# Kernel tuning notes

Hardware: AMD Instinct MI355X
Metric: run time of the kernel (lower is better)

Reference implementation:

```python
import jax, jax.numpy as jnp
import numpy as np

N_NODES = 100000
N_EDGES = 1600000
D_NODE = 96
D_EDGE = 32
N_GRAPHS = 128
BN_EPS = 1e-5


def setup_inputs() -> dict:
    key = jax.random.key(0)
    ks = jax.random.split(key, 8)
    x = jax.random.normal(ks[0], (N_NODES, D_NODE), dtype=jnp.float32)
    edge_attr = jax.random.normal(ks[1], (N_EDGES, D_EDGE), dtype=jnp.float32)
    edge_index = jax.random.randint(ks[2], (2, N_EDGES), 0, N_NODES, dtype=jnp.int64)
    batch = jnp.sort(jax.random.randint(ks[3], (N_NODES,), 0, N_GRAPHS, dtype=jnp.int64))
    W1 = jax.random.normal(ks[4], (16, D_NODE + D_EDGE), dtype=jnp.float32) * 0.09
    b1 = jax.random.normal(ks[5], (16,), dtype=jnp.float32) * 0.01
    gamma = jnp.ones((16,), dtype=jnp.float32)
    beta = jnp.zeros((16,), dtype=jnp.float32)
    run_mean = jnp.zeros((16,), dtype=jnp.float32)
    run_var = jnp.ones((16,), dtype=jnp.float32)
    W2 = jax.random.normal(ks[6], (1, 16), dtype=jnp.float32) * 0.25
    b2 = jax.random.normal(ks[7], (1,), dtype=jnp.float32) * 0.01
    return {"x": x, "edge_attr": edge_attr, "edge_index": edge_index, "batch": batch,
            "W1": W1, "b1": b1, "gamma": gamma, "beta": beta,
            "run_mean": run_mean, "run_var": run_var, "W2": W2, "b2": b2}


def reference(x, edge_attr, edge_index, batch, W1, b1, gamma, beta, run_mean, run_var, W2, b2):
    src, dst = edge_index[0], edge_index[1]
    # per-edge message: MLP(cat([x_j, edge_attr]))  -- [E, d_node+d_edge]
    msg_in = jnp.concatenate([x[src], edge_attr], axis=1)
    h = msg_in @ W1.T + b1                                  # [E, 16]
    # BatchNorm1d in eval mode (running stats); Dropout is identity in eval
    h = gamma * (h - run_mean) * jax.lax.rsqrt(run_var + BN_EPS) + beta
    h = jax.nn.relu(h)
    msg = h @ W2.T + b2                                     # [E, 1]
    # scatter-add messages to target nodes
    node_out = jax.ops.segment_sum(msg, dst, num_segments=N_NODES)   # [N, 1]
    # global add pool per graph
    pooled = jax.ops.segment_sum(node_out, batch, num_segments=N_GRAPHS)  # [G, 1]
    # mean over feature dim (size 1)
    return jnp.mean(pooled, axis=1)                         # [G]
```

## Files before the change

### kernel.cpp

```cpp
#include <hip/hip_runtime.h>

#define N_NODES 100000
#define N_EDGES 1600000
#define D_NODE 96
#define D_EDGE 32
#define N_GRAPHS 128
#define BN_EPS 1e-5f

#define EDGE_BLOCKS 1024
#define EDGE_THREADS 256

__global__ void prep_kernel(const float* __restrict__ W1, const float* __restrict__ b1,
                            const float* __restrict__ gamma, const float* __restrict__ beta,
                            const float* __restrict__ rmean, const float* __restrict__ rvar,
                            const float* __restrict__ W2, const float* __restrict__ b2,
                            float* __restrict__ w1n, float* __restrict__ w1e,
                            float* __restrict__ cw) {
    int t = threadIdx.x;
    if (t < 16) {
        float A = gamma[t] * rsqrtf(rvar[t] + BN_EPS);
        cw[t] = A * (b1[t] - rmean[t]) + beta[t];
        cw[16 + t] = W2[t];
        for (int j = 0; j < D_NODE; ++j)
            w1n[t * D_NODE + j] = A * W1[t * (D_NODE + D_EDGE) + j];
        for (int j = 0; j < D_EDGE; ++j)
            w1e[t * D_EDGE + j] = A * W1[t * (D_NODE + D_EDGE) + D_NODE + j];
    }
    if (t == 16) cw[32] = b2[0];
}

__global__ __launch_bounds__(256) void node_proj_kernel(const float* __restrict__ x,
                                                        const float* __restrict__ w1n,
                                                        float* __restrict__ y) {
    int n = blockIdx.x * 256 + threadIdx.x;
    if (n >= N_NODES) return;
    const float4* xr = (const float4*)(x + (size_t)n * D_NODE);
    float acc[16];
#pragma unroll
    for (int k = 0; k < 16; ++k) acc[k] = 0.f;
#pragma unroll
    for (int j4 = 0; j4 < D_NODE / 4; ++j4) {
        float4 xv = xr[j4];
#pragma unroll
        for (int k = 0; k < 16; ++k) {
            const float* w = w1n + k * D_NODE + j4 * 4;
            acc[k] += xv.x * w[0] + xv.y * w[1] + xv.z * w[2] + xv.w * w[3];
        }
    }
    float4* yr = (float4*)(y + (size_t)n * 16);
#pragma unroll
    for (int q = 0; q < 4; ++q)
        yr[q] = make_float4(acc[q * 4 + 0], acc[q * 4 + 1], acc[q * 4 + 2], acc[q * 4 + 3]);
}

__global__ __launch_bounds__(EDGE_THREADS) void edge_kernel(
    const float* __restrict__ ea, const int* __restrict__ eidx,
    const int* __restrict__ batch, const float* __restrict__ y,
    const float* __restrict__ w1e, const float* __restrict__ cw,
    float* __restrict__ partials) {
    __shared__ float bins[N_GRAPHS];
    int t = threadIdx.x;
    if (t < N_GRAPHS) bins[t] = 0.f;
    __syncthreads();

    const int* srcp = eidx;
    const int* dstp = eidx + N_EDGES;
    float b2v = cw[32];

    for (int e = blockIdx.x * EDGE_THREADS + t; e < N_EDGES; e += EDGE_BLOCKS * EDGE_THREADS) {
        int s = srcp[e];
        int d = dstp[e];

        const float4* er = (const float4*)(ea + (size_t)e * D_EDGE);
        float4 ev[8];
#pragma unroll
        for (int i = 0; i < 8; ++i) ev[i] = er[i];

        float ya[16];
        const float4* yr = (const float4*)(y + (size_t)s * 16);
#pragma unroll
        for (int q = 0; q < 4; ++q) ((float4*)ya)[q] = yr[q];

        float msg = b2v;
#pragma unroll
        for (int k = 0; k < 16; ++k) {
            float z = 0.f;
#pragma unroll
            for (int i = 0; i < 8; ++i) {
                const float* w = w1e + k * D_EDGE + i * 4;
                z += ev[i].x * w[0] + ev[i].y * w[1] + ev[i].z * w[2] + ev[i].w * w[3];
            }
            float h = z + ya[k] + cw[k];
            msg += fmaxf(h, 0.f) * cw[16 + k];
        }

        int g = batch[d];
        atomicAdd(&bins[g], msg);
    }

    __syncthreads();
    if (t < N_GRAPHS) partials[(size_t)blockIdx.x * N_GRAPHS + t] = bins[t];
}

__global__ __launch_bounds__(256) void reduce_kernel(const float* __restrict__ partials,
                                                     float* __restrict__ out) {
    __shared__ float s[256];
    int g = blockIdx.x;
    float acc = 0.f;
    for (int b = threadIdx.x; b < EDGE_BLOCKS; b += 256)
        acc += partials[(size_t)b * N_GRAPHS + g];
    s[threadIdx.x] = acc;
    __syncthreads();
    for (int w = 128; w > 0; w >>= 1) {
        if (threadIdx.x < w) s[threadIdx.x] += s[threadIdx.x + w];
        __syncthreads();
    }
    if (threadIdx.x == 0) out[g] = s[0];
}

extern "C" void kernel_launch(void* const* d_in, const int* in_sizes, int n_in,
                              void* d_out, int out_size, void* d_ws, size_t ws_size,
                              hipStream_t stream) {
    const float* x     = (const float*)d_in[0];
    const float* ea    = (const float*)d_in[1];
    const int*   eidx  = (const int*)d_in[2];
    const int*   batch = (const int*)d_in[3];
    const float* W1    = (const float*)d_in[4];
    const float* b1    = (const float*)d_in[5];
    const float* gamma = (const float*)d_in[6];
    const float* beta  = (const float*)d_in[7];
    const float* rmean = (const float*)d_in[8];
    const float* rvar  = (const float*)d_in[9];
    const float* W2    = (const float*)d_in[10];
    const float* b2    = (const float*)d_in[11];
    float* out = (float*)d_out;

    float* ws = (float*)d_ws;
    float* w1n      = ws;
    float* w1e      = ws + 1536;
    float* cw       = ws + 2048;
    float* y        = ws + 4096;
    float* partials = ws + 4096 + (size_t)N_NODES * 16;

    prep_kernel<<<1, 64, 0, stream>>>(W1, b1, gamma, beta, rmean, rvar, W2, b2, w1n, w1e, cw);
    node_proj_kernel<<<(N_NODES + 255) / 256, 256, 0, stream>>>(x, w1n, y);
    edge_kernel<<<EDGE_BLOCKS, EDGE_THREADS, 0, stream>>>(ea, eidx, batch, y, w1e, cw, partials);
    reduce_kernel<<<N_GRAPHS, 256, 0, stream>>>(partials, out);
}
```

Before: 392.7 us.

## Store node projections in bf16, stage weights in LDS, parallelize prep

Node projections are now stored as packed bf16, which halves the random-gather traffic in the edge kernel, and are unpacked with shifts. Both the node and edge kernels copy their weight matrices and constants into shared memory and use explicit FMAs. The prep kernel is spread over many threads instead of 16 serial loops. The bf16 rounding of projections adds numerical error to the per-edge pre-activations.

After: 427.4 us. 8.8% more time.

```diff
diff --git a/kernel.cpp b/kernel.cpp
--- a/kernel.cpp
+++ b/kernel.cpp
@@ -1,4 +1,5 @@
 #include <hip/hip_runtime.h>
+#include <hip/hip_bf16.h>
 
 #define N_NODES 100000
 #define N_EDGES 1600000
@@ -10,30 +11,53 @@
 #define EDGE_BLOCKS 1024
 #define EDGE_THREADS 256
 
-__global__ void prep_kernel(const float* __restrict__ W1, const float* __restrict__ b1,
-                            const float* __restrict__ gamma, const float* __restrict__ beta,
-                            const float* __restrict__ rmean, const float* __restrict__ rvar,
-                            const float* __restrict__ W2, const float* __restrict__ b2,
-                            float* __restrict__ w1n, float* __restrict__ w1e,
-                            float* __restrict__ cw) {
-    int t = threadIdx.x;
-    if (t < 16) {
-        float A = gamma[t] * rsqrtf(rvar[t] + BN_EPS);
-        cw[t] = A * (b1[t] - rmean[t]) + beta[t];
-        cw[16 + t] = W2[t];
-        for (int j = 0; j < D_NODE; ++j)
-            w1n[t * D_NODE + j] = A * W1[t * (D_NODE + D_EDGE) + j];
-        for (int j = 0; j < D_EDGE; ++j)
-            w1e[t * D_EDGE + j] = A * W1[t * (D_NODE + D_EDGE) + D_NODE + j];
+static __device__ __forceinline__ unsigned short f2bf(float f) {
+    __hip_bfloat16 h = __float2bfloat16(f);
+    return *reinterpret_cast<unsigned short*>(&h);
+}
+static __device__ __forceinline__ void unpack_bf16x2(unsigned u, float& lo, float& hi) {
+    lo = __uint_as_float(u << 16);
+    hi = __uint_as_float(u & 0xFFFF0000u);
+}
+
+__global__ __launch_bounds__(256) void prep_kernel(
+    const float* __restrict__ W1, const float* __restrict__ b1,
+    const float* __restrict__ gamma, const float* __restrict__ beta,
+    const float* __restrict__ rmean, const float* __restrict__ rvar,
+    const float* __restrict__ W2, const float* __restrict__ b2,
+    float* __restrict__ w1n, float* __restrict__ w1e, float* __restrict__ cw) {
+    int idx = blockIdx.x * 256 + threadIdx.x;
+    if (idx < 1536) {
+        int k = idx / 96, j = idx % 96;
+        float A = gamma[k] * rsqrtf(rvar[k] + BN_EPS);
+        w1n[idx] = A * W1[k * (D_NODE + D_EDGE) + j];
+    } else if (idx < 2048) {
+        int r = idx - 1536;
+        int k = r / 32, j = r % 32;
+        float A = gamma[k] * rsqrtf(rvar[k] + BN_EPS);
+        w1e[r] = A * W1[k * (D_NODE + D_EDGE) + D_NODE + j];
+    } else if (idx < 2064) {
+        int k = idx - 2048;
+        float A = gamma[k] * rsqrtf(rvar[k] + BN_EPS);
+        cw[k] = A * (b1[k] - rmean[k]) + beta[k];
+    } else if (idx < 2080) {
+        int k = idx - 2064;
+        cw[16 + k] = W2[k];
+    } else if (idx == 2080) {
+        cw[32] = b2[0];
     }
-    if (t == 16) cw[32] = b2[0];
 }
 
 __global__ __launch_bounds__(256) void node_proj_kernel(const float* __restrict__ x,
                                                         const float* __restrict__ w1n,
-                                                        float* __restrict__ y) {
+                                                        unsigned short* __restrict__ y) {
+    __shared__ __align__(16) float sw[16 * 96];
+    for (int i = threadIdx.x; i < 16 * 96; i += 256) sw[i] = w1n[i];
+    __syncthreads();
+
     int n = blockIdx.x * 256 + threadIdx.x;
     if (n >= N_NODES) return;
+
     const float4* xr = (const float4*)(x + (size_t)n * D_NODE);
     float acc[16];
 #pragma unroll
@@ -43,29 +67,38 @@
         float4 xv = xr[j4];
 #pragma unroll
         for (int k = 0; k < 16; ++k) {
-            const float* w = w1n + k * D_NODE + j4 * 4;
-            acc[k] += xv.x * w[0] + xv.y * w[1] + xv.z * w[2] + xv.w * w[3];
+            float4 w = *(const float4*)&sw[k * 96 + j4 * 4];
+            acc[k] = fmaf(xv.x, w.x, acc[k]);
+            acc[k] = fmaf(xv.y, w.y, acc[k]);
+            acc[k] = fmaf(xv.z, w.z, acc[k]);
+            acc[k] = fmaf(xv.w, w.w, acc[k]);
         }
     }
-    float4* yr = (float4*)(y + (size_t)n * 16);
+    unsigned w[8];
 #pragma unroll
-    for (int q = 0; q < 4; ++q)
-        yr[q] = make_float4(acc[q * 4 + 0], acc[q * 4 + 1], acc[q * 4 + 2], acc[q * 4 + 3]);
+    for (int i = 0; i < 8; ++i)
+        w[i] = (unsigned)f2bf(acc[2 * i]) | ((unsigned)f2bf(acc[2 * i + 1]) << 16);
+    uint4* yr = (uint4*)(y + (size_t)n * 16);
+    yr[0] = make_uint4(w[0], w[1], w[2], w[3]);
+    yr[1] = make_uint4(w[4], w[5], w[6], w[7]);
 }
 
 __global__ __launch_bounds__(EDGE_THREADS) void edge_kernel(
     const float* __restrict__ ea, const int* __restrict__ eidx,
-    const int* __restrict__ batch, const float* __restrict__ y,
+    const int* __restrict__ batch, const unsigned short* __restrict__ y,
     const float* __restrict__ w1e, const float* __restrict__ cw,
     float* __restrict__ partials) {
+    __shared__ __align__(16) float sw[16 * 32];
+    __shared__ float scw[33];
     __shared__ float bins[N_GRAPHS];
     int t = threadIdx.x;
+    for (int i = t; i < 16 * 32; i += EDGE_THREADS) sw[i] = w1e[i];
+    if (t < 33) scw[t] = cw[t];
     if (t < N_GRAPHS) bins[t] = 0.f;
     __syncthreads();
 
     const int* srcp = eidx;
     const int* dstp = eidx + N_EDGES;
-    float b2v = cw[32];
 
     for (int e = blockIdx.x * EDGE_THREADS + t; e < N_EDGES; e += EDGE_BLOCKS * EDGE_THREADS) {
         int s = srcp[e];
@@ -76,22 +109,33 @@
 #pragma unroll
         for (int i = 0; i < 8; ++i) ev[i] = er[i];
 
+        const uint4* yrow = (const uint4*)(y + (size_t)s * 16);
+        uint4 y0 = yrow[0], y1 = yrow[1];
         float ya[16];
-        const float4* yr = (const float4*)(y + (size_t)s * 16);
-#pragma unroll
-        for (int q = 0; q < 4; ++q) ((float4*)ya)[q] = yr[q];
+        unpack_bf16x2(y0.x, ya[0], ya[1]);
+        unpack_bf16x2(y0.y, ya[2], ya[3]);
+        unpack_bf16x2(y0.z, ya[4], ya[5]);
+        unpack_bf16x2(y0.w, ya[6], ya[7]);
+        unpack_bf16x2(y1.x, ya[8], ya[9]);
+        unpack_bf16x2(y1.y, ya[10], ya[11]);
+        unpack_bf16x2(y1.z, ya[12], ya[13]);
+        unpack_bf16x2(y1.w, ya[14], ya[15]);
 
-        float msg = b2v;
+        float msg = scw[32];
 #pragma unroll
         for (int k = 0; k < 16; ++k) {
+            const float4* wr = (const float4*)&sw[k * 32];
             float z = 0.f;
 #pragma unroll
             for (int i = 0; i < 8; ++i) {
-                const float* w = w1e + k * D_EDGE + i * 4;
-                z += ev[i].x * w[0] + ev[i].y * w[1] + ev[i].z * w[2] + ev[i].w * w[3];
+                float4 w = wr[i];
+                z = fmaf(ev[i].x, w.x, z);
+                z = fmaf(ev[i].y, w.y, z);
+                z = fmaf(ev[i].z, w.z, z);
+                z = fmaf(ev[i].w, w.w, z);
             }
-            float h = z + ya[k] + cw[k];
-            msg += fmaxf(h, 0.f) * cw[16 + k];
+            float h = z + ya[k] + scw[k];
+            msg = fmaf(fmaxf(h, 0.f), scw[16 + k], msg);
         }
 
         int g = batch[d];
@@ -136,13 +180,13 @@
     float* out = (float*)d_out;
 
     float* ws = (float*)d_ws;
-    float* w1n      = ws;
-    float* w1e      = ws + 1536;
-    float* cw       = ws + 2048;
-    float* y        = ws + 4096;
-    float* partials = ws + 4096 + (size_t)N_NODES * 16;
+    float*          w1n      = ws;
+    float*          w1e      = ws + 1536;
+    float*          cw       = ws + 2048;
+    unsigned short* y        = (unsigned short*)(ws + 4096);
+    float*          partials = ws + 4096 + 800000;
 
-    prep_kernel<<<1, 64, 0, stream>>>(W1, b1, gamma, beta, rmean, rvar, W2, b2, w1n, w1e, cw);
+    prep_kernel<<<9, 256, 0, stream>>>(W1, b1, gamma, beta, rmean, rvar, W2, b2, w1n, w1e, cw);
     node_proj_kernel<<<(N_NODES + 255) / 256, 256, 0, stream>>>(x, w1n, y);
     edge_kernel<<<EDGE_BLOCKS, EDGE_THREADS, 0, stream>>>(ea, eidx, batch, y, w1e, cw, partials);
     reduce_kernel<<<N_GRAPHS, 256, 0, stream>>>(partials, out);
```
